# Kernel optimization log

Measured on AMD Instinct MI355X. Metric: run time of the kernel, lower is better.

Reference implementation:

```python
import jax, jax.numpy as jnp
import numpy as np


def setup_inputs() -> dict:
    key = jax.random.key(0)
    kq, kk, kv = jax.random.split(key, 3)
    B, S, D = 32, 2048, 128
    q = jax.random.normal(kq, (B, S, D), dtype=jnp.float32)
    k = jax.random.normal(kk, (B, S, D), dtype=jnp.float32)
    v = jax.random.normal(kv, (B, S, D), dtype=jnp.float32)
    return {"q": q, "k": k, "v": v}


def reference(q, k, v):
    # scaled = exp(QK^T / sqrt(d_k)); attn = scaled / sum(scaled) ; out = attn @ V
    # (softmax computed via raw exp/sum, matching the original module; no mask,
    #  dropout is identity in eval mode)
    d_k = q.shape[2]
    scale = 1.0 / jnp.sqrt(jnp.asarray(d_k, dtype=q.dtype))
    scores = jnp.einsum("bqd,bkd->bqk", q, k) * scale  # [B, S, S]
    e = jnp.exp(scores)
    attn = e / jnp.sum(e, axis=-1, keepdims=True)
    return jnp.einsum("bqk,bkd->bqd", attn, v)
```

## Files before the change

### kernel.cpp

```cpp
#include <hip/hip_runtime.h>
#include <hip/hip_bf16.h>
#include <stdint.h>

typedef __attribute__((ext_vector_type(8))) __bf16 bf16x8;
typedef __attribute__((ext_vector_type(4))) float  f32x4;
typedef __attribute__((ext_vector_type(2))) unsigned int u32x2;

#define S_  2048
#define D_  128
#define QB  128
#define KB  32
#define NT  (S_/KB)
#define VPANEL 1056
#define VBUF   (8*VPANEL)

__device__ __forceinline__ __bf16 f2bf(float f){ return (__bf16)f; }

__device__ __forceinline__ bf16x8 pack8(float4 a, float4 b){
  bf16x8 r;
  r[0]=f2bf(a.x); r[1]=f2bf(a.y); r[2]=f2bf(a.z); r[3]=f2bf(a.w);
  r[4]=f2bf(b.x); r[5]=f2bf(b.y); r[6]=f2bf(b.z); r[7]=f2bf(b.w);
  return r;
}

__global__ __launch_bounds__(256, 2)
void attn_fwd(const float* __restrict__ Q, const float* __restrict__ K,
              const float* __restrict__ V, float* __restrict__ O) {
  __shared__ __align__(128) __bf16 k_lds[3][KB][136];
  __shared__ __align__(128) unsigned char v_raw[3][VBUF];

  const int t   = threadIdx.x;
  const int w   = t >> 6;
  const int l   = t & 63;
  const int l16 = l & 15;
  const int lg  = l >> 4;

  const int f  = blockIdx.x;
  const int b  = ((f & 7) << 2) | ((f >> 3) & 3);
  const int bq = f >> 5;

  const float* Qb = Q + (size_t)b * (S_*D_);
  const float* Kb = K + (size_t)b * (S_*D_);
  const float* Vb = V + (size_t)b * (S_*D_);
  float*       Ob = O + (size_t)b * (S_*D_);

  const int q0 = bq*QB + w*32;
  const float scale = 0.08838834764831845f;

  bf16x8 qf[2][4];
  #pragma unroll
  for (int qt=0; qt<2; ++qt){
    const float* qr = Qb + (size_t)(q0 + qt*16 + l16) * D_;
    #pragma unroll
    for (int ds=0; ds<4; ++ds){
      const float4* p = (const float4*)(qr + ds*32 + lg*8);
      float4 a = p[0], c = p[1];
      a.x*=scale; a.y*=scale; a.z*=scale; a.w*=scale;
      c.x*=scale; c.y*=scale; c.z*=scale; c.w*=scale;
      qf[qt][ds] = pack8(a, c);
    }
  }

  f32x4 acc[2][8];
  #pragma unroll
  for (int qt=0; qt<2; ++qt)
    #pragma unroll
    for (int dt=0; dt<8; ++dt)
      acc[qt][dt] = (f32x4){0.f,0.f,0.f,0.f};
  float den0 = 0.f, den1 = 0.f;

  const int sr  = t >> 3;
  const int sdt = t & 7;
  const int par = sdt & 1;
  const float* Kst = Kb + (size_t)sr * D_ + sdt*16;
  const float* Vst = Vb + (size_t)sr * D_ + sdt*16;

  float4 kst0,kst1,kst2,kst3, vst0,vst1,vst2,vst3;

  #define LOADT(IT) do { \
    const float4* kp_ = (const float4*)(Kst + (size_t)(IT)*KB*D_); \
    const float4* vp_ = (const float4*)(Vst + (size_t)(IT)*KB*D_); \
    kst0=kp_[0]; kst1=kp_[1]; kst2=kp_[2]; kst3=kp_[3]; \
    vst0=vp_[0]; vst1=vp_[1]; vst2=vp_[2]; vst3=vp_[3]; \
  } while(0)

  #define WRITET(BUF) do { \
    *(bf16x8*)&k_lds[BUF][sr][sdt*16    ] = pack8(kst0,kst1); \
    *(bf16x8*)&k_lds[BUF][sr][sdt*16 + 8] = pack8(kst2,kst3); \
    unsigned char* vb_ = &v_raw[BUF][sdt*VPANEL + sr*32]; \
    *(bf16x8*)(vb_ + (par<<4))        = pack8(vst0,vst1); \
    *(bf16x8*)(vb_ + ((par^1)<<4))    = pack8(vst2,vst3); \
  } while(0)

  const unsigned vbase  = (unsigned)(uintptr_t)&v_raw[0][0];
  const unsigned troff_e = (unsigned)(lg*128 + (l16>>2)*32 + ((l16&3)*8));
  const unsigned troff_o = (unsigned)(lg*128 + (l16>>2)*32 + (((l16&3)*8) ^ 16));

  LOADT(0); WRITET(0); LOADT(1);
  __syncthreads();

  int cur = 0, nxt = 1, nn = 2;
  for (int it = 0; it < NT; ++it){
    if (it+1 < NT) WRITET(nxt);
    if (it+2 < NT) LOADT(it+2);

    f32x4 s[2][2];
    #pragma unroll
    for (int ct=0; ct<2; ++ct){
      bf16x8 kf[4];
      #pragma unroll
      for (int ds=0; ds<4; ++ds)
        kf[ds] = *(const bf16x8*)&k_lds[cur][ct*16 + l16][ds*32 + lg*8];
      #pragma unroll
      for (int qt=0; qt<2; ++qt){
        f32x4 sv = (f32x4){0.f,0.f,0.f,0.f};
        #pragma unroll
        for (int ds=0; ds<4; ++ds)
          sv = __builtin_amdgcn_mfma_f32_16x16x32_bf16(kf[ds], qf[qt][ds], sv, 0,0,0);
        s[qt][ct] = sv;
      }
    }

    u32x2 vlo[8], vhi[8];
    {
      const unsigned vb_e = vbase + (unsigned)(cur*VBUF) + troff_e;
      const unsigned vb_o = vbase + (unsigned)(cur*VBUF) + troff_o;
      #pragma unroll
      for (int dt=0; dt<8; ++dt){
        const unsigned a = ((dt & 1) ? vb_o : vb_e) + (unsigned)(dt*VPANEL);
        asm volatile("ds_read_b64_tr_b16 %0, %2\n\t"
                     "ds_read_b64_tr_b16 %1, %2 offset:512"
                     : "=&v"(vlo[dt]), "=&v"(vhi[dt])
                     : "v"(a));
      }
    }

    bf16x8 pf[2];
    #pragma unroll
    for (int qt=0; qt<2; ++qt){
      float dsum = 0.f;
      #pragma unroll
      for (int ct=0; ct<2; ++ct){
        #pragma unroll
        for (int r=0; r<4; ++r){
          float e = __expf(s[qt][ct][r]);
          dsum += e;
          pf[qt][ct*4+r] = f2bf(e);
        }
      }
      if (qt==0) den0 += dsum; else den1 += dsum;
    }

    asm volatile("s_waitcnt lgkmcnt(0)" ::: "memory");
    __builtin_amdgcn_sched_barrier(0);

    #pragma unroll
    for (int dt=0; dt<8; ++dt){
      union { bf16x8 v; u32x2 u[2]; } uu;
      uu.u[0] = vlo[dt]; uu.u[1] = vhi[dt];
      acc[0][dt] = __builtin_amdgcn_mfma_f32_16x16x32_bf16(uu.v, pf[0], acc[0][dt], 0,0,0);
      acc[1][dt] = __builtin_amdgcn_mfma_f32_16x16x32_bf16(uu.v, pf[1], acc[1][dt], 0,0,0);
    }

    __syncthreads();
    int tmp = cur; cur = nxt; nxt = nn; nn = tmp;
  }

  #pragma unroll
  for (int qt=0; qt<2; ++qt){
    float dsum = (qt==0) ? den0 : den1;
    dsum += __shfl_xor(dsum, 16);
    dsum += __shfl_xor(dsum, 32);
    const float inv = 1.0f / dsum;
    float* orow = Ob + (size_t)(q0 + qt*16 + l16) * D_ + lg*4;
    #pragma unroll
    for (int dt=0; dt<8; ++dt){
      f32x4 a4 = acc[qt][dt];
      float4 o4;
      o4.x = a4[0]*inv; o4.y = a4[1]*inv; o4.z = a4[2]*inv; o4.w = a4[3]*inv;
      *(float4*)(orow + dt*16) = o4;
    }
  }
}

extern "C" void kernel_launch(void* const* d_in, const int* in_sizes, int n_in,
                              void* d_out, int out_size, void* d_ws, size_t ws_size,
                              hipStream_t stream) {
  const float* q = (const float*)d_in[0];
  const float* k = (const float*)d_in[1];
  const float* v = (const float*)d_in[2];
  float* o = (float*)d_out;
  attn_fwd<<<dim3(512), dim3(256), 0, stream>>>(q, k, v, o);
}
```

Baseline: 95.24 us.

## Double the key tile to 64 and switch from triple to double LDS buffering

Raises the K/V tile per iteration from 32 to 64 rows, processed as two 32-row halves, and drops from three LDS buffers to two. This halves the number of __syncthreads barriers and loop iterations, with each thread loading twice as much K/V data per prefetch. The costs are more staging registers, which could add spills or hurt occupancy at two blocks per CU, and a larger LDS footprint per buffer.

Result: slower. 136.0 us (+42.9%).

```diff
diff --git a/kernel.cpp b/kernel.cpp
--- a/kernel.cpp
+++ b/kernel.cpp
@@ -9,9 +9,9 @@
 #define S_  2048
 #define D_  128
 #define QB  128
-#define KB  32
+#define KB  64
 #define NT  (S_/KB)
-#define VPANEL 1056
+#define VPANEL 2080
 #define VBUF   (8*VPANEL)
 
 __device__ __forceinline__ __bf16 f2bf(float f){ return (__bf16)f; }
@@ -26,8 +26,8 @@
 __global__ __launch_bounds__(256, 2)
 void attn_fwd(const float* __restrict__ Q, const float* __restrict__ K,
               const float* __restrict__ V, float* __restrict__ O) {
-  __shared__ __align__(128) __bf16 k_lds[3][KB][136];
-  __shared__ __align__(128) unsigned char v_raw[3][VBUF];
+  __shared__ __align__(128) __bf16 k_lds[2][KB][136];
+  __shared__ __align__(128) unsigned char v_raw[2][VBUF];
 
   const int t   = threadIdx.x;
   const int w   = t >> 6;
@@ -75,21 +75,31 @@
   const float* Kst = Kb + (size_t)sr * D_ + sdt*16;
   const float* Vst = Vb + (size_t)sr * D_ + sdt*16;
 
-  float4 kst0,kst1,kst2,kst3, vst0,vst1,vst2,vst3;
+  float4 ksta0,ksta1,ksta2,ksta3, kstb0,kstb1,kstb2,kstb3;
+  float4 vsta0,vsta1,vsta2,vsta3, vstb0,vstb1,vstb2,vstb3;
 
   #define LOADT(IT) do { \
-    const float4* kp_ = (const float4*)(Kst + (size_t)(IT)*KB*D_); \
-    const float4* vp_ = (const float4*)(Vst + (size_t)(IT)*KB*D_); \
-    kst0=kp_[0]; kst1=kp_[1]; kst2=kp_[2]; kst3=kp_[3]; \
-    vst0=vp_[0]; vst1=vp_[1]; vst2=vp_[2]; vst3=vp_[3]; \
+    const float4* ka_ = (const float4*)(Kst + (size_t)(IT)*KB*D_); \
+    const float4* kb_ = (const float4*)(Kst + (size_t)(IT)*KB*D_ + 32*D_); \
+    const float4* va_ = (const float4*)(Vst + (size_t)(IT)*KB*D_); \
+    const float4* vb2_ = (const float4*)(Vst + (size_t)(IT)*KB*D_ + 32*D_); \
+    ksta0=ka_[0]; ksta1=ka_[1]; ksta2=ka_[2]; ksta3=ka_[3]; \
+    kstb0=kb_[0]; kstb1=kb_[1]; kstb2=kb_[2]; kstb3=kb_[3]; \
+    vsta0=va_[0]; vsta1=va_[1]; vsta2=va_[2]; vsta3=va_[3]; \
+    vstb0=vb2_[0]; vstb1=vb2_[1]; vstb2=vb2_[2]; vstb3=vb2_[3]; \
   } while(0)
 
   #define WRITET(BUF) do { \
-    *(bf16x8*)&k_lds[BUF][sr][sdt*16    ] = pack8(kst0,kst1); \
-    *(bf16x8*)&k_lds[BUF][sr][sdt*16 + 8] = pack8(kst2,kst3); \
-    unsigned char* vb_ = &v_raw[BUF][sdt*VPANEL + sr*32]; \
-    *(bf16x8*)(vb_ + (par<<4))        = pack8(vst0,vst1); \
-    *(bf16x8*)(vb_ + ((par^1)<<4))    = pack8(vst2,vst3); \
+    *(bf16x8*)&k_lds[BUF][sr][sdt*16    ]     = pack8(ksta0,ksta1); \
+    *(bf16x8*)&k_lds[BUF][sr][sdt*16 + 8]     = pack8(ksta2,ksta3); \
+    *(bf16x8*)&k_lds[BUF][sr+32][sdt*16    ]  = pack8(kstb0,kstb1); \
+    *(bf16x8*)&k_lds[BUF][sr+32][sdt*16 + 8]  = pack8(kstb2,kstb3); \
+    unsigned char* va_p = &v_raw[BUF][sdt*VPANEL + sr*32]; \
+    *(bf16x8*)(va_p + (par<<4))          = pack8(vsta0,vsta1); \
+    *(bf16x8*)(va_p + ((par^1)<<4))      = pack8(vsta2,vsta3); \
+    unsigned char* vb_p = va_p + 32*32; \
+    *(bf16x8*)(vb_p + (par<<4))          = pack8(vstb0,vstb1); \
+    *(bf16x8*)(vb_p + ((par^1)<<4))      = pack8(vstb2,vstb3); \
   } while(0)
 
   const unsigned vbase  = (unsigned)(uintptr_t)&v_raw[0][0];
@@ -99,71 +109,74 @@
   LOADT(0); WRITET(0); LOADT(1);
   __syncthreads();
 
-  int cur = 0, nxt = 1, nn = 2;
   for (int it = 0; it < NT; ++it){
-    if (it+1 < NT) WRITET(nxt);
+    const int cur = it & 1;
+    if (it+1 < NT) WRITET(cur^1);
     if (it+2 < NT) LOADT(it+2);
 
-    f32x4 s[2][2];
-    #pragma unroll
-    for (int ct=0; ct<2; ++ct){
-      bf16x8 kf[4];
+    #pragma unroll
+    for (int h = 0; h < 2; ++h){
+      f32x4 s[2][2];
       #pragma unroll
-      for (int ds=0; ds<4; ++ds)
-        kf[ds] = *(const bf16x8*)&k_lds[cur][ct*16 + l16][ds*32 + lg*8];
+      for (int c2=0; c2<2; ++c2){
+        const int ct = 2*h + c2;
+        bf16x8 kf[4];
+        #pragma unroll
+        for (int ds=0; ds<4; ++ds)
+          kf[ds] = *(const bf16x8*)&k_lds[cur][ct*16 + l16][ds*32 + lg*8];
+        #pragma unroll
+        for (int qt=0; qt<2; ++qt){
+          f32x4 sv = (f32x4){0.f,0.f,0.f,0.f};
+          #pragma unroll
+          for (int ds=0; ds<4; ++ds)
+            sv = __builtin_amdgcn_mfma_f32_16x16x32_bf16(kf[ds], qf[qt][ds], sv, 0,0,0);
+          s[qt][c2] = sv;
+        }
+      }
+
+      u32x2 vlo[8], vhi[8];
+      {
+        const unsigned vb_e = vbase + (unsigned)(cur*VBUF) + (unsigned)(h*1024) + troff_e;
+        const unsigned vb_o = vbase + (unsigned)(cur*VBUF) + (unsigned)(h*1024) + troff_o;
+        #pragma unroll
+        for (int dt=0; dt<8; ++dt){
+          const unsigned a = ((dt & 1) ? vb_o : vb_e) + (unsigned)(dt*VPANEL);
+          asm volatile("ds_read_b64_tr_b16 %0, %2\n\t"
+                       "ds_read_b64_tr_b16 %1, %2 offset:512"
+                       : "=&v"(vlo[dt]), "=&v"(vhi[dt])
+                       : "v"(a));
+        }
+      }
+
+      bf16x8 pf[2];
       #pragma unroll
       for (int qt=0; qt<2; ++qt){
-        f32x4 sv = (f32x4){0.f,0.f,0.f,0.f};
-        #pragma unroll
-        for (int ds=0; ds<4; ++ds)
-          sv = __builtin_amdgcn_mfma_f32_16x16x32_bf16(kf[ds], qf[qt][ds], sv, 0,0,0);
-        s[qt][ct] = sv;
-      }
-    }
-
-    u32x2 vlo[8], vhi[8];
-    {
-      const unsigned vb_e = vbase + (unsigned)(cur*VBUF) + troff_e;
-      const unsigned vb_o = vbase + (unsigned)(cur*VBUF) + troff_o;
+        float dsum = 0.f;
+        #pragma unroll
+        for (int c2=0; c2<2; ++c2){
+          #pragma unroll
+          for (int r=0; r<4; ++r){
+            float e = __expf(s[qt][c2][r]);
+            dsum += e;
+            pf[qt][c2*4+r] = f2bf(e);
+          }
+        }
+        if (qt==0) den0 += dsum; else den1 += dsum;
+      }
+
+      asm volatile("s_waitcnt lgkmcnt(0)" ::: "memory");
+      __builtin_amdgcn_sched_barrier(0);
+
       #pragma unroll
       for (int dt=0; dt<8; ++dt){
-        const unsigned a = ((dt & 1) ? vb_o : vb_e) + (unsigned)(dt*VPANEL);
-        asm volatile("ds_read_b64_tr_b16 %0, %2\n\t"
-                     "ds_read_b64_tr_b16 %1, %2 offset:512"
-                     : "=&v"(vlo[dt]), "=&v"(vhi[dt])
-                     : "v"(a));
+        union { bf16x8 v; u32x2 u[2]; } uu;
+        uu.u[0] = vlo[dt]; uu.u[1] = vhi[dt];
+        acc[0][dt] = __builtin_amdgcn_mfma_f32_16x16x32_bf16(uu.v, pf[0], acc[0][dt], 0,0,0);
+        acc[1][dt] = __builtin_amdgcn_mfma_f32_16x16x32_bf16(uu.v, pf[1], acc[1][dt], 0,0,0);
       }
     }
 
-    bf16x8 pf[2];
-    #pragma unroll
-    for (int qt=0; qt<2; ++qt){
-      float dsum = 0.f;
-      #pragma unroll
-      for (int ct=0; ct<2; ++ct){
-        #pragma unroll
-        for (int r=0; r<4; ++r){
-          float e = __expf(s[qt][ct][r]);
-          dsum += e;
-          pf[qt][ct*4+r] = f2bf(e);
-        }
-      }
-      if (qt==0) den0 += dsum; else den1 += dsum;
-    }
-
-    asm volatile("s_waitcnt lgkmcnt(0)" ::: "memory");
-    __builtin_amdgcn_sched_barrier(0);
-
-    #pragma unroll
-    for (int dt=0; dt<8; ++dt){
-      union { bf16x8 v; u32x2 u[2]; } uu;
-      uu.u[0] = vlo[dt]; uu.u[1] = vhi[dt];
-      acc[0][dt] = __builtin_amdgcn_mfma_f32_16x16x32_bf16(uu.v, pf[0], acc[0][dt], 0,0,0);
-      acc[1][dt] = __builtin_amdgcn_mfma_f32_16x16x32_bf16(uu.v, pf[1], acc[1][dt], 0,0,0);
-    }
-
     __syncthreads();
-    int tmp = cur; cur = nxt; nxt = nn; nn = tmp;
   }
 
   #pragma unroll
```

## Halve waves per block, give each wave 64 query rows, double-buffer LDS

Applied to the files above, without the earlier changes.

Each block now runs 2 waves of 128 threads instead of 4, and each wave handles 64 query rows instead of 32. Every K/V fragment read from LDS therefore feeds twice as many MFMAs, and each thread stages two rows of K and V per tile. LDS buffering drops from triple to double to shrink shared memory. The cost is far more registers per thread (acc grows to 128 floats plus Q fragments) and fewer waves on the GPU to hide latency, with launch bounds set to 1 block per CU.

Result: slower. 110.7 us (+16.3%).

```diff
diff --git a/kernel.cpp b/kernel.cpp
--- a/kernel.cpp
+++ b/kernel.cpp
@@ -23,11 +23,11 @@
   return r;
 }
 
-__global__ __launch_bounds__(256, 2)
+__global__ __launch_bounds__(128, 1)
 void attn_fwd(const float* __restrict__ Q, const float* __restrict__ K,
               const float* __restrict__ V, float* __restrict__ O) {
-  __shared__ __align__(128) __bf16 k_lds[3][KB][136];
-  __shared__ __align__(128) unsigned char v_raw[3][VBUF];
+  __shared__ __align__(128) __bf16 k_lds[2][KB][136];
+  __shared__ __align__(128) unsigned char v_raw[2][VBUF];
 
   const int t   = threadIdx.x;
   const int w   = t >> 6;
@@ -44,12 +44,12 @@
   const float* Vb = V + (size_t)b * (S_*D_);
   float*       Ob = O + (size_t)b * (S_*D_);
 
-  const int q0 = bq*QB + w*32;
+  const int q0 = bq*QB + w*64;
   const float scale = 0.08838834764831845f;
 
-  bf16x8 qf[2][4];
+  bf16x8 qf[4][4];
   #pragma unroll
-  for (int qt=0; qt<2; ++qt){
+  for (int qt=0; qt<4; ++qt){
     const float* qr = Qb + (size_t)(q0 + qt*16 + l16) * D_;
     #pragma unroll
     for (int ds=0; ds<4; ++ds){
@@ -61,13 +61,13 @@
     }
   }
 
-  f32x4 acc[2][8];
+  f32x4 acc[4][8];
   #pragma unroll
-  for (int qt=0; qt<2; ++qt)
+  for (int qt=0; qt<4; ++qt)
     #pragma unroll
     for (int dt=0; dt<8; ++dt)
       acc[qt][dt] = (f32x4){0.f,0.f,0.f,0.f};
-  float den0 = 0.f, den1 = 0.f;
+  float den[4] = {0.f, 0.f, 0.f, 0.f};
 
   const int sr  = t >> 3;
   const int sdt = t & 7;
@@ -75,36 +75,46 @@
   const float* Kst = Kb + (size_t)sr * D_ + sdt*16;
   const float* Vst = Vb + (size_t)sr * D_ + sdt*16;
 
-  float4 kst0,kst1,kst2,kst3, vst0,vst1,vst2,vst3;
+  float4 ksa0,ksa1,ksa2,ksa3, ksb0,ksb1,ksb2,ksb3;
+  float4 vsa0,vsa1,vsa2,vsa3, vsb0,vsb1,vsb2,vsb3;
 
   #define LOADT(IT) do { \
-    const float4* kp_ = (const float4*)(Kst + (size_t)(IT)*KB*D_); \
-    const float4* vp_ = (const float4*)(Vst + (size_t)(IT)*KB*D_); \
-    kst0=kp_[0]; kst1=kp_[1]; kst2=kp_[2]; kst3=kp_[3]; \
-    vst0=vp_[0]; vst1=vp_[1]; vst2=vp_[2]; vst3=vp_[3]; \
+    const float4* ka_ = (const float4*)(Kst + (size_t)(IT)*KB*D_); \
+    const float4* kb_ = (const float4*)(Kst + (size_t)(IT)*KB*D_ + 16*D_); \
+    const float4* va_ = (const float4*)(Vst + (size_t)(IT)*KB*D_); \
+    const float4* vb2_ = (const float4*)(Vst + (size_t)(IT)*KB*D_ + 16*D_); \
+    ksa0=ka_[0]; ksa1=ka_[1]; ksa2=ka_[2]; ksa3=ka_[3]; \
+    ksb0=kb_[0]; ksb1=kb_[1]; ksb2=kb_[2]; ksb3=kb_[3]; \
+    vsa0=va_[0]; vsa1=va_[1]; vsa2=va_[2]; vsa3=va_[3]; \
+    vsb0=vb2_[0]; vsb1=vb2_[1]; vsb2=vb2_[2]; vsb3=vb2_[3]; \
   } while(0)
 
   #define WRITET(BUF) do { \
-    *(bf16x8*)&k_lds[BUF][sr][sdt*16    ] = pack8(kst0,kst1); \
-    *(bf16x8*)&k_lds[BUF][sr][sdt*16 + 8] = pack8(kst2,kst3); \
-    unsigned char* vb_ = &v_raw[BUF][sdt*VPANEL + sr*32]; \
-    *(bf16x8*)(vb_ + (par<<4))        = pack8(vst0,vst1); \
-    *(bf16x8*)(vb_ + ((par^1)<<4))    = pack8(vst2,vst3); \
+    *(bf16x8*)&k_lds[BUF][sr][sdt*16    ]     = pack8(ksa0,ksa1); \
+    *(bf16x8*)&k_lds[BUF][sr][sdt*16 + 8]     = pack8(ksa2,ksa3); \
+    *(bf16x8*)&k_lds[BUF][sr+16][sdt*16    ]  = pack8(ksb0,ksb1); \
+    *(bf16x8*)&k_lds[BUF][sr+16][sdt*16 + 8]  = pack8(ksb2,ksb3); \
+    unsigned char* va_p = &v_raw[BUF][sdt*VPANEL + sr*32]; \
+    *(bf16x8*)(va_p + (par<<4))          = pack8(vsa0,vsa1); \
+    *(bf16x8*)(va_p + ((par^1)<<4))      = pack8(vsa2,vsa3); \
+    unsigned char* vb_p = va_p + 16*32; \
+    *(bf16x8*)(vb_p + (par<<4))          = pack8(vsb0,vsb1); \
+    *(bf16x8*)(vb_p + ((par^1)<<4))      = pack8(vsb2,vsb3); \
   } while(0)
 
-  const unsigned vbase  = (unsigned)(uintptr_t)&v_raw[0][0];
+  const unsigned vbase   = (unsigned)(uintptr_t)&v_raw[0][0];
   const unsigned troff_e = (unsigned)(lg*128 + (l16>>2)*32 + ((l16&3)*8));
   const unsigned troff_o = (unsigned)(lg*128 + (l16>>2)*32 + (((l16&3)*8) ^ 16));
 
   LOADT(0); WRITET(0); LOADT(1);
   __syncthreads();
 
-  int cur = 0, nxt = 1, nn = 2;
   for (int it = 0; it < NT; ++it){
-    if (it+1 < NT) WRITET(nxt);
+    const int cur = it & 1;
+    if (it+1 < NT) WRITET(cur^1);
     if (it+2 < NT) LOADT(it+2);
 
-    f32x4 s[2][2];
+    f32x4 s[4][2];
     #pragma unroll
     for (int ct=0; ct<2; ++ct){
       bf16x8 kf[4];
@@ -112,7 +122,7 @@
       for (int ds=0; ds<4; ++ds)
         kf[ds] = *(const bf16x8*)&k_lds[cur][ct*16 + l16][ds*32 + lg*8];
       #pragma unroll
-      for (int qt=0; qt<2; ++qt){
+      for (int qt=0; qt<4; ++qt){
         f32x4 sv = (f32x4){0.f,0.f,0.f,0.f};
         #pragma unroll
         for (int ds=0; ds<4; ++ds)
@@ -135,9 +145,9 @@
       }
     }
 
-    bf16x8 pf[2];
-    #pragma unroll
-    for (int qt=0; qt<2; ++qt){
+    bf16x8 pf[4];
+    #pragma unroll
+    for (int qt=0; qt<4; ++qt){
       float dsum = 0.f;
       #pragma unroll
       for (int ct=0; ct<2; ++ct){
@@ -148,7 +158,7 @@
           pf[qt][ct*4+r] = f2bf(e);
         }
       }
-      if (qt==0) den0 += dsum; else den1 += dsum;
+      den[qt] += dsum;
     }
 
     asm volatile("s_waitcnt lgkmcnt(0)" ::: "memory");
@@ -158,17 +168,17 @@
     for (int dt=0; dt<8; ++dt){
       union { bf16x8 v; u32x2 u[2]; } uu;
       uu.u[0] = vlo[dt]; uu.u[1] = vhi[dt];
-      acc[0][dt] = __builtin_amdgcn_mfma_f32_16x16x32_bf16(uu.v, pf[0], acc[0][dt], 0,0,0);
-      acc[1][dt] = __builtin_amdgcn_mfma_f32_16x16x32_bf16(uu.v, pf[1], acc[1][dt], 0,0,0);
+      #pragma unroll
+      for (int qt=0; qt<4; ++qt)
+        acc[qt][dt] = __builtin_amdgcn_mfma_f32_16x16x32_bf16(uu.v, pf[qt], acc[qt][dt], 0,0,0);
     }
 
     __syncthreads();
-    int tmp = cur; cur = nxt; nxt = nn; nn = tmp;
   }
 
   #pragma unroll
-  for (int qt=0; qt<2; ++qt){
-    float dsum = (qt==0) ? den0 : den1;
+  for (int qt=0; qt<4; ++qt){
+    float dsum = den[qt];
     dsum += __shfl_xor(dsum, 16);
     dsum += __shfl_xor(dsum, 32);
     const float inv = 1.0f / dsum;
@@ -190,5 +200,5 @@
   const float* k = (const float*)d_in[1];
   const float* v = (const float*)d_in[2];
   float* o = (float*)d_out;
-  attn_fwd<<<dim3(512), dim3(256), 0, stream>>>(q, k, v, o);
+  attn_fwd<<<dim3(512), dim3(128), 0, stream>>>(q, k, v, o);
 }
```

## Software-pipeline PV matmul one tile behind QK and shrink LDS to double buffers

Applied to the files above, without the earlier changes.

Restructures the main loop so the PV MFMA for tile i-1 runs while the QK MFMA and exp for tile i are in flight. It uses V fragments and probabilities carried in registers across iterations, with a prologue and an epilogue PV. LDS buffering drops from triple to double, which lowers shared memory per block. The cost is more live registers (vlo/vhi/pf held across the barrier), which may raise register pressure at two blocks per CU. The barrier count per iteration is unchanged.

Result: no change. 94.66 us (-0.6%).

```diff
diff --git a/kernel.cpp b/kernel.cpp
--- a/kernel.cpp
+++ b/kernel.cpp
@@ -26,8 +26,8 @@
 __global__ __launch_bounds__(256, 2)
 void attn_fwd(const float* __restrict__ Q, const float* __restrict__ K,
               const float* __restrict__ V, float* __restrict__ O) {
-  __shared__ __align__(128) __bf16 k_lds[3][KB][136];
-  __shared__ __align__(128) unsigned char v_raw[3][VBUF];
+  __shared__ __align__(128) __bf16 k_lds[2][KB][136];
+  __shared__ __align__(128) unsigned char v_raw[2][VBUF];
 
   const int t   = threadIdx.x;
   const int w   = t >> 6;
@@ -92,79 +92,104 @@
     *(bf16x8*)(vb_ + ((par^1)<<4))    = pack8(vst2,vst3); \
   } while(0)
 
-  const unsigned vbase  = (unsigned)(uintptr_t)&v_raw[0][0];
+  const unsigned vbase   = (unsigned)(uintptr_t)&v_raw[0][0];
   const unsigned troff_e = (unsigned)(lg*128 + (l16>>2)*32 + ((l16&3)*8));
   const unsigned troff_o = (unsigned)(lg*128 + (l16>>2)*32 + (((l16&3)*8) ^ 16));
 
+  u32x2 vlo[8], vhi[8];
+  bf16x8 pf[2];
+
+  #define QK_BLOCK(CUR, SVAR) do { \
+    _Pragma("unroll") \
+    for (int ct=0; ct<2; ++ct){ \
+      bf16x8 kf[4]; \
+      _Pragma("unroll") \
+      for (int ds=0; ds<4; ++ds) \
+        kf[ds] = *(const bf16x8*)&k_lds[CUR][ct*16 + l16][ds*32 + lg*8]; \
+      _Pragma("unroll") \
+      for (int qt=0; qt<2; ++qt){ \
+        f32x4 sv = (f32x4){0.f,0.f,0.f,0.f}; \
+        _Pragma("unroll") \
+        for (int ds=0; ds<4; ++ds) \
+          sv = __builtin_amdgcn_mfma_f32_16x16x32_bf16(kf[ds], qf[qt][ds], sv, 0,0,0); \
+        SVAR[qt][ct] = sv; \
+      } \
+    } \
+  } while(0)
+
+  #define PV_BLOCK() do { \
+    _Pragma("unroll") \
+    for (int dt=0; dt<8; ++dt){ \
+      union { bf16x8 v; u32x2 u[2]; } uu; \
+      uu.u[0] = vlo[dt]; uu.u[1] = vhi[dt]; \
+      acc[0][dt] = __builtin_amdgcn_mfma_f32_16x16x32_bf16(uu.v, pf[0], acc[0][dt], 0,0,0); \
+      acc[1][dt] = __builtin_amdgcn_mfma_f32_16x16x32_bf16(uu.v, pf[1], acc[1][dt], 0,0,0); \
+    } \
+  } while(0)
+
+  #define EXP_BLOCK(SVAR) do { \
+    _Pragma("unroll") \
+    for (int qt=0; qt<2; ++qt){ \
+      float dsum = 0.f; \
+      _Pragma("unroll") \
+      for (int ct=0; ct<2; ++ct){ \
+        _Pragma("unroll") \
+        for (int r=0; r<4; ++r){ \
+          float e = __expf(SVAR[qt][ct][r]); \
+          dsum += e; \
+          pf[qt][ct*4+r] = f2bf(e); \
+        } \
+      } \
+      if (qt==0) den0 += dsum; else den1 += dsum; \
+    } \
+  } while(0)
+
+  #define TR_ISSUE(CUR) do { \
+    const unsigned vb_e = vbase + (unsigned)((CUR)*VBUF) + troff_e; \
+    const unsigned vb_o = vbase + (unsigned)((CUR)*VBUF) + troff_o; \
+    _Pragma("unroll") \
+    for (int dt=0; dt<8; ++dt){ \
+      const unsigned a = ((dt & 1) ? vb_o : vb_e) + (unsigned)(dt*VPANEL); \
+      asm volatile("ds_read_b64_tr_b16 %0, %2\n\t" \
+                   "ds_read_b64_tr_b16 %1, %2 offset:512" \
+                   : "=&v"(vlo[dt]), "=&v"(vhi[dt]) \
+                   : "v"(a)); \
+    } \
+  } while(0)
+
+  #define FENCE() do { \
+    asm volatile("s_waitcnt lgkmcnt(0)" ::: "memory"); \
+    __builtin_amdgcn_sched_barrier(0); \
+    __syncthreads(); \
+  } while(0)
+
   LOADT(0); WRITET(0); LOADT(1);
   __syncthreads();
 
-  int cur = 0, nxt = 1, nn = 2;
-  for (int it = 0; it < NT; ++it){
-    if (it+1 < NT) WRITET(nxt);
+  {
+    WRITET(1);
+    LOADT(2);
+    f32x4 s0[2][2];
+    QK_BLOCK(0, s0);
+    EXP_BLOCK(s0);
+    TR_ISSUE(0);
+    FENCE();
+  }
+
+  for (int it = 1; it < NT; ++it){
+    const int cur = it & 1;
+    if (it+1 < NT) WRITET(cur^1);
     if (it+2 < NT) LOADT(it+2);
 
     f32x4 s[2][2];
-    #pragma unroll
-    for (int ct=0; ct<2; ++ct){
-      bf16x8 kf[4];
-      #pragma unroll
-      for (int ds=0; ds<4; ++ds)
-        kf[ds] = *(const bf16x8*)&k_lds[cur][ct*16 + l16][ds*32 + lg*8];
-      #pragma unroll
-      for (int qt=0; qt<2; ++qt){
-        f32x4 sv = (f32x4){0.f,0.f,0.f,0.f};
-        #pragma unroll
-        for (int ds=0; ds<4; ++ds)
-          sv = __builtin_amdgcn_mfma_f32_16x16x32_bf16(kf[ds], qf[qt][ds], sv, 0,0,0);
-        s[qt][ct] = sv;
-      }
-    }
-
-    u32x2 vlo[8], vhi[8];
-    {
-      const unsigned vb_e = vbase + (unsigned)(cur*VBUF) + troff_e;
-      const unsigned vb_o = vbase + (unsigned)(cur*VBUF) + troff_o;
-      #pragma unroll
-      for (int dt=0; dt<8; ++dt){
-        const unsigned a = ((dt & 1) ? vb_o : vb_e) + (unsigned)(dt*VPANEL);
-        asm volatile("ds_read_b64_tr_b16 %0, %2\n\t"
-                     "ds_read_b64_tr_b16 %1, %2 offset:512"
-                     : "=&v"(vlo[dt]), "=&v"(vhi[dt])
-                     : "v"(a));
-      }
-    }
-
-    bf16x8 pf[2];
-    #pragma unroll
-    for (int qt=0; qt<2; ++qt){
-      float dsum = 0.f;
-      #pragma unroll
-      for (int ct=0; ct<2; ++ct){
-        #pragma unroll
-        for (int r=0; r<4; ++r){
-          float e = __expf(s[qt][ct][r]);
-          dsum += e;
-          pf[qt][ct*4+r] = f2bf(e);
-        }
-      }
-      if (qt==0) den0 += dsum; else den1 += dsum;
-    }
-
-    asm volatile("s_waitcnt lgkmcnt(0)" ::: "memory");
-    __builtin_amdgcn_sched_barrier(0);
-
-    #pragma unroll
-    for (int dt=0; dt<8; ++dt){
-      union { bf16x8 v; u32x2 u[2]; } uu;
-      uu.u[0] = vlo[dt]; uu.u[1] = vhi[dt];
-      acc[0][dt] = __builtin_amdgcn_mfma_f32_16x16x32_bf16(uu.v, pf[0], acc[0][dt], 0,0,0);
-      acc[1][dt] = __builtin_amdgcn_mfma_f32_16x16x32_bf16(uu.v, pf[1], acc[1][dt], 0,0,0);
-    }
-
-    __syncthreads();
-    int tmp = cur; cur = nxt; nxt = nn; nn = tmp;
-  }
+    QK_BLOCK(cur, s);
+    PV_BLOCK();
+    EXP_BLOCK(s);
+    TR_ISSUE(cur);
+    FENCE();
+  }
+
+  PV_BLOCK();
 
   #pragma unroll
   for (int qt=0; qt<2; ++qt){
```
